# Kernel optimization log

Measured on AMD Instinct MI355X. Metric: run time of the kernel, lower is better.

## Reference

```python
import jax, jax.numpy as jnp
import numpy as np

B, T, J, D = 32, 1024, 128, 256

def setup_inputs() -> dict:
    key = jax.random.key(0)
    k1, k2, k3 = jax.random.split(key, 3)
    C = jax.random.normal(k1, (B, T, D), dtype=jnp.float32)
    Q = jax.random.normal(k2, (B, J, D), dtype=jnp.float32)
    w = jax.random.uniform(k3, (3 * D,), dtype=jnp.float32)  # torch.rand(d_model*3)
    return {"C": C, "Q": Q, "w": w}


def reference(C, Q, w):
    d = C.shape[-1]
    # AttentionFlowLayer: w^T [h; u; h*u] computed as streaming weighted sum
    # (avoids materializing the (b,t,j,3d) concat tensor; same math)
    w_h, w_u, w_hu = w[:d], w[d:2 * d], w[2 * d:]
    S = ((C @ w_h)[:, :, None]                         # (b,t,1)
         + (Q @ w_u)[:, None, :]                       # (b,1,j)
         + jnp.einsum('btd,bjd->btj', C * w_hu, Q))    # (b,t,j)

    S_j = jax.nn.softmax(S, axis=2)  # softmax over query dim j
    S_t = jax.nn.softmax(S, axis=1)  # softmax over context dim t

    # Context2Query
    A = jnp.einsum('btj,bjd->btd', S_j, Q)
    # DCNAttention: S_j @ S_t^T @ C, associated as S_j @ (S_t^T @ C) for efficiency
    tmp = jnp.einsum('bsj,bsd->bjd', S_t, C)           # (b,j,d)
    Bm = jnp.einsum('btj,bjd->btd', S_j, tmp)          # (b,t,d)

    # droprate = 0.0 -> dropout is identity
    return jnp.concatenate((C, A, C * A, C * Bm), axis=2)  # (b,t,4d)
```

## Files before the change

kernel.cpp:

```cpp
#include <hip/hip_runtime.h>
#include <math.h>

#define BB 32
#define TT 1024
#define JJ 128
#define DD 256

typedef unsigned short u16;
typedef short s16x8 __attribute__((ext_vector_type(8)));
typedef float f32x4 __attribute__((ext_vector_type(4)));

#define MFMA_BF16(a, b, c) __builtin_amdgcn_mfma_f32_16x16x32_bf16((a), (b), (c), 0, 0, 0)

__device__ inline u16 f2bf(float f) {
    unsigned int u = __float_as_uint(f);
    u += 0x7FFFu + ((u >> 16) & 1u);
    return (u16)(u >> 16);
}
__device__ inline float bf2f(u16 h) {
    return __uint_as_float(((unsigned int)h) << 16);
}

__global__ __launch_bounds__(256) void k_qprep(const float* __restrict__ Q,
                                               const float* __restrict__ w,
                                               float* __restrict__ qu,
                                               u16* __restrict__ Qhi,
                                               u16* __restrict__ Qlo,
                                               u16* __restrict__ Qt) {
    const int b = blockIdx.x >> 1, jh = blockIdx.x & 1;
    const int tid = threadIdx.x;
    __shared__ float sW[256];
    __shared__ __align__(16) u16 sTr[256 * 72];
    sW[tid] = w[DD + tid];
    __syncthreads();
    const int jj = tid >> 2, s = tid & 3;
    const int j = jh * 64 + jj;
    const float* qp = Q + ((size_t)b * JJ + j) * DD + s * 64;
    u16* hp = Qhi + ((size_t)b * JJ + j) * DD + s * 64;
    u16* lp = Qlo + ((size_t)b * JJ + j) * DD + s * 64;
    float dot = 0.f;
    #pragma unroll
    for (int q = 0; q < 16; q++) {
        float4 v = *(const float4*)(qp + q * 4);
        const float* wq = &sW[s * 64 + q * 4];
        dot += v.x * wq[0] + v.y * wq[1] + v.z * wq[2] + v.w * wq[3];
        ushort4 h, l;
        h.x = f2bf(v.x); l.x = f2bf(v.x - bf2f(h.x));
        h.y = f2bf(v.y); l.y = f2bf(v.y - bf2f(h.y));
        h.z = f2bf(v.z); l.z = f2bf(v.z - bf2f(h.z));
        h.w = f2bf(v.w); l.w = f2bf(v.w - bf2f(h.w));
        *(ushort4*)(hp + q * 4) = h;
        *(ushort4*)(lp + q * 4) = l;
        int d = s * 64 + q * 4;
        sTr[(d + 0) * 72 + jj] = h.x;
        sTr[(d + 1) * 72 + jj] = h.y;
        sTr[(d + 2) * 72 + jj] = h.z;
        sTr[(d + 3) * 72 + jj] = h.w;
    }
    dot += __shfl_xor(dot, 1, 64);
    dot += __shfl_xor(dot, 2, 64);
    if (s == 0) qu[b * JJ + j] = dot;
    __syncthreads();
    const u16* srow = &sTr[tid * 72];
    u16* drow = &Qt[((size_t)b * DD + tid) * JJ + jh * 64];
    #pragma unroll
    for (int q = 0; q < 8; q++) *(uint4*)&drow[q * 8] = *(const uint4*)&srow[q * 8];
}

__global__ __launch_bounds__(256) void k_S(const float* __restrict__ C,
                                           const u16* __restrict__ Qhi,
                                           const u16* __restrict__ Qlo,
                                           const float* __restrict__ w,
                                           const float* __restrict__ qu,
                                           u16* __restrict__ Xg,
                                           u16* __restrict__ Xt,
                                           u16* __restrict__ Cbf,
                                           float* __restrict__ rowmax,
                                           float* __restrict__ rowrcp,
                                           float* __restrict__ pm,
                                           float* __restrict__ ps) {
    const int id = blockIdx.x;
    const int b  = id & 31;
    const int bx = id >> 5;
    const int t0 = bx * 64;
    const int tid = threadIdx.x;

    union SMem {
        struct { u16 Ah[64 * 72]; u16 Al[64 * 72]; u16 Bh[128 * 72]; u16 Bl[128 * 72]; } g;
        struct { float S[64 * 132]; float RM[64]; float W[4]; float ER[64]; float PS2[256]; } e;
    };
    __shared__ __align__(16) SMem sm;
    __shared__ float sCH[64];
    __shared__ float sQU[128];

    if (tid < 128) sQU[tid] = qu[b * JJ + tid];

    const float* whu = w + 2 * DD;
    const float* Cb  = C + ((size_t)b * TT + t0) * DD;

    const int lane = tid & 63, wv = tid >> 6;
    const int wm = wv >> 1, wn = wv & 1;
    const int lr = lane & 15, lg = lane >> 4;

    f32x4 zero4 = {0.f, 0.f, 0.f, 0.f};
    f32x4 acc[2][4];
    #pragma unroll
    for (int m = 0; m < 2; m++)
        #pragma unroll
        for (int n = 0; n < 4; n++) acc[m][n] = zero4;

    const int tA = tid >> 2, sA = (tid & 3) * 16;
    const int jB = tid >> 1, sB = (tid & 1) * 32;
    float chdot = 0.f;

    for (int kc = 0; kc < DD; kc += 64) {
        __syncthreads();
        {
            const float* cp  = Cb + (size_t)tA * DD + kc + sA;
            const float* wp  = whu + kc + sA;
            const float* whp = w + kc + sA;
            float cc[16], ww[16], wh[16];
            #pragma unroll
            for (int q = 0; q < 4; q++) {
                *(float4*)&cc[q * 4] = *(const float4*)(cp + q * 4);
                *(float4*)&ww[q * 4] = *(const float4*)(wp + q * 4);
                *(float4*)&wh[q * 4] = *(const float4*)(whp + q * 4);
            }
            u16 hi16[16], lo16[16], cb16[16];
            #pragma unroll
            for (int u = 0; u < 16; u++) {
                chdot += cc[u] * wh[u];
                cb16[u] = f2bf(cc[u]);
                float v = cc[u] * ww[u];
                u16 h = f2bf(v);
                hi16[u] = h;
                lo16[u] = f2bf(v - bf2f(h));
            }
            u16* cbp = &Cbf[((size_t)b * TT + t0 + tA) * DD + kc + sA];
            *(uint4*)&cbp[0] = *(uint4*)&cb16[0];
            *(uint4*)&cbp[8] = *(uint4*)&cb16[8];
            int o = tA * 72 + sA;
            *(uint4*)&sm.g.Ah[o]     = *(uint4*)&hi16[0];
            *(uint4*)&sm.g.Ah[o + 8] = *(uint4*)&hi16[8];
            *(uint4*)&sm.g.Al[o]     = *(uint4*)&lo16[0];
            *(uint4*)&sm.g.Al[o + 8] = *(uint4*)&lo16[8];
        }
        {
            const uint4* qh = (const uint4*)&Qhi[((size_t)b * JJ + jB) * DD + kc + sB];
            const uint4* ql = (const uint4*)&Qlo[((size_t)b * JJ + jB) * DD + kc + sB];
            uint4* dh = (uint4*)&sm.g.Bh[jB * 72 + sB];
            uint4* dl = (uint4*)&sm.g.Bl[jB * 72 + sB];
            #pragma unroll
            for (int q = 0; q < 4; q++) { dh[q] = qh[q]; dl[q] = ql[q]; }
        }
        __syncthreads();
        #pragma unroll
        for (int ks = 0; ks < 2; ks++) {
            const int ko = ks * 32 + lg * 8;
            s16x8 ah[2], al[2], bh[4], bl[4];
            #pragma unroll
            for (int m = 0; m < 2; m++) {
                ah[m] = *(const s16x8*)&sm.g.Ah[(wm * 32 + m * 16 + lr) * 72 + ko];
                al[m] = *(const s16x8*)&sm.g.Al[(wm * 32 + m * 16 + lr) * 72 + ko];
            }
            #pragma unroll
            for (int n = 0; n < 4; n++) {
                bh[n] = *(const s16x8*)&sm.g.Bh[(wn * 64 + n * 16 + lr) * 72 + ko];
                bl[n] = *(const s16x8*)&sm.g.Bl[(wn * 64 + n * 16 + lr) * 72 + ko];
            }
            #pragma unroll
            for (int m = 0; m < 2; m++)
                #pragma unroll
                for (int n = 0; n < 4; n++) {
                    f32x4 t = acc[m][n];
                    t = MFMA_BF16(ah[m], bh[n], t);
                    t = MFMA_BF16(ah[m], bl[n], t);
                    t = MFMA_BF16(al[m], bh[n], t);
                    acc[m][n] = t;
                }
        }
    }

    chdot += __shfl_xor(chdot, 1, 64);
    chdot += __shfl_xor(chdot, 2, 64);
    if ((tid & 3) == 0) sCH[tid >> 2] = chdot;

    __syncthreads();
    #pragma unroll
    for (int m = 0; m < 2; m++) {
        int row0 = wm * 32 + m * 16 + lg * 4;
        #pragma unroll
        for (int n = 0; n < 4; n++) {
            int col = wn * 64 + n * 16 + lr;
            float qv = sQU[col];
            #pragma unroll
            for (int reg = 0; reg < 4; reg++)
                sm.e.S[(row0 + reg) * 132 + col] = acc[m][n][reg] + sCH[row0 + reg] + qv;
        }
    }
    __syncthreads();
    {
        int r = tid >> 2, s = tid & 3;
        float v[32];
        float* Sr = &sm.e.S[r * 132 + s * 32];
        #pragma unroll
        for (int q = 0; q < 8; q++) *(float4*)&v[q * 4] = *(const float4*)&Sr[q * 4];
        float mx = v[0];
        #pragma unroll
        for (int u = 1; u < 32; u++) mx = fmaxf(mx, v[u]);
        mx = fmaxf(mx, __shfl_xor(mx, 1, 64));
        mx = fmaxf(mx, __shfl_xor(mx, 2, 64));
        float sum = 0.f;
        #pragma unroll
        for (int u = 0; u < 32; u++) { v[u] = __expf(v[u] - mx); sum += v[u]; }
        sum += __shfl_xor(sum, 1, 64);
        sum += __shfl_xor(sum, 2, 64);
        #pragma unroll
        for (int q = 0; q < 8; q++) *(float4*)&Sr[q * 4] = *(const float4*)&v[q * 4];
        u16 xp[32];
        #pragma unroll
        for (int u = 0; u < 32; u++) xp[u] = f2bf(v[u]);
        u16* xgp = &Xg[((size_t)b * TT + t0 + r) * JJ + s * 32];
        #pragma unroll
        for (int q = 0; q < 4; q++) *(uint4*)&xgp[q * 8] = *(uint4*)&xp[q * 8];
        if (s == 0) {
            sm.e.RM[r] = mx;
            rowmax[(size_t)b * TT + t0 + r] = mx;
            rowrcp[(size_t)b * TT + t0 + r] = 1.0f / sum;
        }
        float wmx = mx;
        wmx = fmaxf(wmx, __shfl_xor(wmx, 4, 64));
        wmx = fmaxf(wmx, __shfl_xor(wmx, 8, 64));
        wmx = fmaxf(wmx, __shfl_xor(wmx, 16, 64));
        wmx = fmaxf(wmx, __shfl_xor(wmx, 32, 64));
        if (lane == 0) sm.e.W[wv] = wmx;
    }
    __syncthreads();
    const float Mb = fmaxf(fmaxf(sm.e.W[0], sm.e.W[1]), fmaxf(sm.e.W[2], sm.e.W[3]));
    if (tid < 64) sm.e.ER[tid] = __expf(sm.e.RM[tid] - Mb);
    {
        int j = tid & 127, seg = tid >> 7;
        u16 xb[32];
        #pragma unroll
        for (int k = 0; k < 32; k++)
            xb[k] = f2bf(sm.e.S[(seg * 32 + k) * 132 + j]);
        u16* xtp = &Xt[((size_t)b * JJ + j) * TT + t0 + seg * 32];
        #pragma unroll
        for (int q = 0; q < 4; q++) *(uint4*)&xtp[q * 8] = *(uint4*)&xb[q * 8];
    }
    __syncthreads();
    {
        int j = tid & 127, h = tid >> 7;
        float cs = 0.f;
        #pragma unroll
        for (int k = 0; k < 32; k++)
            cs = fmaf(sm.e.S[(h * 32 + k) * 132 + j], sm.e.ER[h * 32 + k], cs);
        sm.e.PS2[h * 128 + j] = cs;
    }
    __syncthreads();
    if (tid < 128) ps[((size_t)b * 16 + bx) * JJ + tid] = sm.e.PS2[tid] + sm.e.PS2[128 + tid];
    if (tid == 0)  pm[b * 16 + bx] = Mb;
}

__global__ __launch_bounds__(256) void k_tmp(const u16* __restrict__ Xt,
                                             const u16* __restrict__ Cbf,
                                             const float* __restrict__ rowmax,
                                             const float* __restrict__ pm,
                                             const float* __restrict__ ps,
                                             u16* __restrict__ Tt) {
    const int id = blockIdx.x;
    const int b = id & 31, dh = id >> 5;
    const int d0 = dh * 32;
    const int tid = threadIdx.x;
    __shared__ __align__(16) u16 sG[128 * 72];
    __shared__ __align__(16) u16 sCt[32 * 72];
    __shared__ float sER[1024];
    __shared__ float sEC[128];
    __shared__ float sPE[16];
    __shared__ float sW2[4];
    const int lane = tid & 63, wv = tid >> 6;

    {
        float4 rm4 = *(const float4*)&rowmax[(size_t)b * TT + tid * 4];
        float km = fmaxf(fmaxf(rm4.x, rm4.y), fmaxf(rm4.z, rm4.w));
        #pragma unroll
        for (int off = 1; off < 64; off <<= 1) km = fmaxf(km, __shfl_xor(km, off, 64));
        if (lane == 0) sW2[wv] = km;
        __syncthreads();
        const float K = fmaxf(fmaxf(sW2[0], sW2[1]), fmaxf(sW2[2], sW2[3]));
        float4 e4;
        e4.x = __expf(rm4.x - K);
        e4.y = __expf(rm4.y - K);
        e4.z = __expf(rm4.z - K);
        e4.w = __expf(rm4.w - K);
        *(float4*)&sER[tid * 4] = e4;
        if (tid < 16) sPE[tid] = __expf(pm[b * 16 + tid] - K);
        __syncthreads();
        if (tid < 128) {
            float cy = 0.f;
            #pragma unroll
            for (int blk = 0; blk < 16; blk++)
                cy = fmaf(ps[((size_t)b * 16 + blk) * JJ + tid], sPE[blk], cy);
            sEC[tid] = 1.0f / cy;
        }
    }

    const int lr = lane & 15, lg = lane >> 4;
    f32x4 zero4 = {0.f, 0.f, 0.f, 0.f};
    f32x4 acc[2][2];
    acc[0][0] = zero4; acc[0][1] = zero4; acc[1][0] = zero4; acc[1][1] = zero4;

    const int gj = tid >> 1, gs = (tid & 1) * 32;
    const int ct = tid & 63, cg = (tid >> 6) * 8;

    for (int tt = 0; tt < TT; tt += 64) {
        __syncthreads();
        {
            const u16* xtp = &Xt[((size_t)b * JJ + gj) * TT + tt + gs];
            u16* gp = &sG[gj * 72 + gs];
            #pragma unroll
            for (int q = 0; q < 4; q++) *(uint4*)&gp[q * 8] = *(const uint4*)&xtp[q * 8];
        }
        {
            float e = sER[tt + ct];
            uint4 cv = *(const uint4*)&Cbf[((size_t)b * TT + tt + ct) * DD + d0 + cg];
            const u16* cp = (const u16*)&cv;
            #pragma unroll
            for (int u = 0; u < 8; u++) sCt[(cg + u) * 72 + ct] = f2bf(bf2f(cp[u]) * e);
        }
        __syncthreads();
        #pragma unroll
        for (int ks = 0; ks < 2; ks++) {
            int ko = ks * 32 + lg * 8;
            s16x8 a0 = *(const s16x8*)&sG[(wv * 32 + lr) * 72 + ko];
            s16x8 a1 = *(const s16x8*)&sG[(wv * 32 + 16 + lr) * 72 + ko];
            s16x8 b0 = *(const s16x8*)&sCt[(lr) * 72 + ko];
            s16x8 b1 = *(const s16x8*)&sCt[(16 + lr) * 72 + ko];
            acc[0][0] = MFMA_BF16(a0, b0, acc[0][0]);
            acc[0][1] = MFMA_BF16(a0, b1, acc[0][1]);
            acc[1][0] = MFMA_BF16(a1, b0, acc[1][0]);
            acc[1][1] = MFMA_BF16(a1, b1, acc[1][1]);
        }
    }
    #pragma unroll
    for (int mr = 0; mr < 2; mr++)
        #pragma unroll
        for (int nr = 0; nr < 2; nr++)
            #pragma unroll
            for (int reg = 0; reg < 4; reg++) {
                int j = wv * 32 + mr * 16 + lg * 4 + reg;
                int d = d0 + nr * 16 + lr;
                Tt[((size_t)b * DD + d) * JJ + j] = f2bf(acc[mr][nr][reg] * sEC[j]);
            }
}

__global__ __launch_bounds__(256) void k_out(const u16* __restrict__ Xg,
                                             const u16* __restrict__ Qt,
                                             const u16* __restrict__ Tt,
                                             const u16* __restrict__ Cbf,
                                             const float* __restrict__ rowrcp,
                                             float* __restrict__ out) {
    const int id = blockIdx.x;
    const int b = id & 31, k = id >> 5;
    const int dc = k & 3, tc = k >> 2;
    const int t0 = tc * 64, d0 = dc * 64;
    const int tid = threadIdx.x;
    __shared__ __align__(16) u16 sX[64 * 136];
    __shared__ __align__(16) u16 sQ[64 * 136];
    __shared__ __align__(16) u16 sT[64 * 136];
    const size_t xbase = ((size_t)b * TT + t0) * JJ;
    const size_t qbase = ((size_t)b * DD + d0) * JJ;
    #pragma unroll
    for (int i = 0; i < 4; i++) {
        int c = tid + 256 * i;
        int row = c >> 4, col = (c & 15) * 8;
        int lo = row * 136 + col;
        *(uint4*)&sX[lo] = *(const uint4*)&Xg[xbase + (size_t)row * JJ + col];
        *(uint4*)&sQ[lo] = *(const uint4*)&Qt[qbase + (size_t)row * JJ + col];
        *(uint4*)&sT[lo] = *(const uint4*)&Tt[qbase + (size_t)row * JJ + col];
    }
    __syncthreads();
    const int lane = tid & 63, wv = tid >> 6;
    const int wm = wv >> 1, wn = wv & 1;
    const int lr = lane & 15, lg = lane >> 4;
    f32x4 zero4 = {0.f, 0.f, 0.f, 0.f};
    f32x4 accA[2][2], accB[2][2];
    #pragma unroll
    for (int mr = 0; mr < 2; mr++)
        #pragma unroll
        for (int nr = 0; nr < 2; nr++) { accA[mr][nr] = zero4; accB[mr][nr] = zero4; }

    #pragma unroll
    for (int ks = 0; ks < 4; ks++) {
        int kc = ks * 32 + lg * 8;
        s16x8 a0 = *(const s16x8*)&sX[(wm * 32 + lr) * 136 + kc];
        s16x8 a1 = *(const s16x8*)&sX[(wm * 32 + 16 + lr) * 136 + kc];
        s16x8 q0 = *(const s16x8*)&sQ[(wn * 32 + lr) * 136 + kc];
        s16x8 q1 = *(const s16x8*)&sQ[(wn * 32 + 16 + lr) * 136 + kc];
        s16x8 u0 = *(const s16x8*)&sT[(wn * 32 + lr) * 136 + kc];
        s16x8 u1 = *(const s16x8*)&sT[(wn * 32 + 16 + lr) * 136 + kc];
        accA[0][0] = MFMA_BF16(a0, q0, accA[0][0]);
        accA[0][1] = MFMA_BF16(a0, q1, accA[0][1]);
        accA[1][0] = MFMA_BF16(a1, q0, accA[1][0]);
        accA[1][1] = MFMA_BF16(a1, q1, accA[1][1]);
        accB[0][0] = MFMA_BF16(a0, u0, accB[0][0]);
        accB[0][1] = MFMA_BF16(a0, u1, accB[0][1]);
        accB[1][0] = MFMA_BF16(a1, u0, accB[1][0]);
        accB[1][1] = MFMA_BF16(a1, u1, accB[1][1]);
    }

    #pragma unroll
    for (int mr = 0; mr < 2; mr++) {
        #pragma unroll
        for (int reg = 0; reg < 4; reg++) {
            int t = t0 + wm * 32 + mr * 16 + lg * 4 + reg;
            float r = rowrcp[(size_t)b * TT + t];
            const u16* Cp = Cbf + ((size_t)b * TT + t) * DD;
            float* op = out + ((size_t)b * TT + t) * (4 * DD);
            #pragma unroll
            for (int nr = 0; nr < 2; nr++) {
                int d = d0 + wn * 32 + nr * 16 + lr;
                float cv = bf2f(Cp[d]);
                float av = accA[mr][nr][reg] * r;
                float bv = accB[mr][nr][reg] * r;
                op[d]          = cv;
                op[DD + d]     = av;
                op[2 * DD + d] = cv * av;
                op[3 * DD + d] = cv * bv;
            }
        }
    }
}

extern "C" void kernel_launch(void* const* d_in, const int* in_sizes, int n_in,
                              void* d_out, int out_size, void* d_ws, size_t ws_size,
                              hipStream_t stream) {
    const float* C = (const float*)d_in[0];
    const float* Q = (const float*)d_in[1];
    const float* w = (const float*)d_in[2];
    float* out = (float*)d_out;
    float* p = (float*)d_ws;

    u16* Xg  = (u16*)p;     p += (size_t)BB * TT * JJ / 2;
    u16* Xt  = (u16*)p;     p += (size_t)BB * JJ * TT / 2;
    u16* Cbf = (u16*)p;     p += (size_t)BB * TT * DD / 2;
    u16* Qt  = (u16*)p;     p += (size_t)BB * DD * JJ / 2;
    u16* Qhi = (u16*)p;     p += (size_t)BB * JJ * DD / 2;
    u16* Qlo = (u16*)p;     p += (size_t)BB * JJ * DD / 2;
    u16* Tt  = (u16*)p;     p += (size_t)BB * DD * JJ / 2;
    float* qu     = p;      p += BB * JJ;
    float* rowmax = p;      p += BB * TT;
    float* rowrcp = p;      p += BB * TT;
    float* pm     = p;      p += BB * 16;
    float* ps     = p;      p += (size_t)BB * 16 * JJ;

    k_qprep <<<dim3(BB * 2), dim3(256), 0, stream>>>(Q, w, qu, Qhi, Qlo, Qt);
    k_S     <<<dim3(16 * BB), dim3(256), 0, stream>>>(C, Qhi, Qlo, w, qu, Xg, Xt, Cbf, rowmax, rowrcp, pm, ps);
    k_tmp   <<<dim3(8 * BB), dim3(256), 0, stream>>>(Xt, Cbf, rowmax, pm, ps, Tt);
    k_out   <<<dim3(64 * BB), dim3(256), 0, stream>>>(Xg, Qt, Tt, Cbf, rowrcp, out);
}
```

Measured before the change: 84.53 us.

## Fuse Q preprocessing kernel into S kernel, recomputing splits per block

Removes the separate k_qprep launch. Each k_S block now loads fp32 Q directly, computes the bf16 hi/lo split and the Q·w_u dot product itself, and blocks with bx==kc/64 write their slice of the transposed bf16 Qt. This saves one kernel launch and the global round-trip of Qhi/Qlo/qu. In exchange every one of the 16 t-blocks per batch redundantly converts the full Q tile and reads fp32 instead of bf16 pairs. The Qt transpose read from LDS is strided and may hit bank conflicts.

```diff
diff --git a/kernel.cpp b/kernel.cpp
--- a/kernel.cpp
+++ b/kernel.cpp
@@ -21,60 +21,13 @@
     return __uint_as_float(((unsigned int)h) << 16);
 }
 
-__global__ __launch_bounds__(256) void k_qprep(const float* __restrict__ Q,
-                                               const float* __restrict__ w,
-                                               float* __restrict__ qu,
-                                               u16* __restrict__ Qhi,
-                                               u16* __restrict__ Qlo,
-                                               u16* __restrict__ Qt) {
-    const int b = blockIdx.x >> 1, jh = blockIdx.x & 1;
-    const int tid = threadIdx.x;
-    __shared__ float sW[256];
-    __shared__ __align__(16) u16 sTr[256 * 72];
-    sW[tid] = w[DD + tid];
-    __syncthreads();
-    const int jj = tid >> 2, s = tid & 3;
-    const int j = jh * 64 + jj;
-    const float* qp = Q + ((size_t)b * JJ + j) * DD + s * 64;
-    u16* hp = Qhi + ((size_t)b * JJ + j) * DD + s * 64;
-    u16* lp = Qlo + ((size_t)b * JJ + j) * DD + s * 64;
-    float dot = 0.f;
-    #pragma unroll
-    for (int q = 0; q < 16; q++) {
-        float4 v = *(const float4*)(qp + q * 4);
-        const float* wq = &sW[s * 64 + q * 4];
-        dot += v.x * wq[0] + v.y * wq[1] + v.z * wq[2] + v.w * wq[3];
-        ushort4 h, l;
-        h.x = f2bf(v.x); l.x = f2bf(v.x - bf2f(h.x));
-        h.y = f2bf(v.y); l.y = f2bf(v.y - bf2f(h.y));
-        h.z = f2bf(v.z); l.z = f2bf(v.z - bf2f(h.z));
-        h.w = f2bf(v.w); l.w = f2bf(v.w - bf2f(h.w));
-        *(ushort4*)(hp + q * 4) = h;
-        *(ushort4*)(lp + q * 4) = l;
-        int d = s * 64 + q * 4;
-        sTr[(d + 0) * 72 + jj] = h.x;
-        sTr[(d + 1) * 72 + jj] = h.y;
-        sTr[(d + 2) * 72 + jj] = h.z;
-        sTr[(d + 3) * 72 + jj] = h.w;
-    }
-    dot += __shfl_xor(dot, 1, 64);
-    dot += __shfl_xor(dot, 2, 64);
-    if (s == 0) qu[b * JJ + j] = dot;
-    __syncthreads();
-    const u16* srow = &sTr[tid * 72];
-    u16* drow = &Qt[((size_t)b * DD + tid) * JJ + jh * 64];
-    #pragma unroll
-    for (int q = 0; q < 8; q++) *(uint4*)&drow[q * 8] = *(const uint4*)&srow[q * 8];
-}
-
 __global__ __launch_bounds__(256) void k_S(const float* __restrict__ C,
-                                           const u16* __restrict__ Qhi,
-                                           const u16* __restrict__ Qlo,
+                                           const float* __restrict__ Q,
                                            const float* __restrict__ w,
-                                           const float* __restrict__ qu,
                                            u16* __restrict__ Xg,
                                            u16* __restrict__ Xt,
                                            u16* __restrict__ Cbf,
+                                           u16* __restrict__ Qt,
                                            float* __restrict__ rowmax,
                                            float* __restrict__ rowrcp,
                                            float* __restrict__ pm,
@@ -93,10 +46,9 @@
     __shared__ float sCH[64];
     __shared__ float sQU[128];
 
-    if (tid < 128) sQU[tid] = qu[b * JJ + tid];
-
     const float* whu = w + 2 * DD;
     const float* Cb  = C + ((size_t)b * TT + t0) * DD;
+    const float* Qb  = Q + (size_t)b * JJ * DD;
 
     const int lane = tid & 63, wv = tid >> 6;
     const int wm = wv >> 1, wn = wv & 1;
@@ -112,6 +64,7 @@
     const int tA = tid >> 2, sA = (tid & 3) * 16;
     const int jB = tid >> 1, sB = (tid & 1) * 32;
     float chdot = 0.f;
+    float qdot  = 0.f;
 
     for (int kc = 0; kc < DD; kc += 64) {
         __syncthreads();
@@ -146,12 +99,26 @@
             *(uint4*)&sm.g.Al[o + 8] = *(uint4*)&lo16[8];
         }
         {
-            const uint4* qh = (const uint4*)&Qhi[((size_t)b * JJ + jB) * DD + kc + sB];
-            const uint4* ql = (const uint4*)&Qlo[((size_t)b * JJ + jB) * DD + kc + sB];
+            const float* qp  = Qb + (size_t)jB * DD + kc + sB;
+            const float* wup = w + DD + kc + sB;
+            float qq[32], wu[32];
+            #pragma unroll
+            for (int q = 0; q < 8; q++) {
+                *(float4*)&qq[q * 4] = *(const float4*)(qp + q * 4);
+                *(float4*)&wu[q * 4] = *(const float4*)(wup + q * 4);
+            }
+            u16 h16[32], l16[32];
+            #pragma unroll
+            for (int u = 0; u < 32; u++) {
+                qdot += qq[u] * wu[u];
+                u16 h = f2bf(qq[u]);
+                h16[u] = h;
+                l16[u] = f2bf(qq[u] - bf2f(h));
+            }
             uint4* dh = (uint4*)&sm.g.Bh[jB * 72 + sB];
             uint4* dl = (uint4*)&sm.g.Bl[jB * 72 + sB];
             #pragma unroll
-            for (int q = 0; q < 4; q++) { dh[q] = qh[q]; dl[q] = ql[q]; }
+            for (int q = 0; q < 4; q++) { dh[q] = *(uint4*)&h16[q * 8]; dl[q] = *(uint4*)&l16[q * 8]; }
         }
         __syncthreads();
         #pragma unroll
@@ -179,11 +146,23 @@
                     acc[m][n] = t;
                 }
         }
+        if (bx == (kc >> 6)) {
+            int dloc = tid >> 2;
+            int j0 = (tid & 3) * 32;
+            u16 qb[32];
+            #pragma unroll
+            for (int u = 0; u < 32; u++) qb[u] = sm.g.Bh[(j0 + u) * 72 + dloc];
+            u16* qtp = &Qt[((size_t)b * DD + kc + dloc) * JJ + j0];
+            #pragma unroll
+            for (int q = 0; q < 4; q++) *(uint4*)&qtp[q * 8] = *(uint4*)&qb[q * 8];
+        }
     }
 
     chdot += __shfl_xor(chdot, 1, 64);
     chdot += __shfl_xor(chdot, 2, 64);
     if ((tid & 3) == 0) sCH[tid >> 2] = chdot;
+    float qd = qdot + __shfl_xor(qdot, 1, 64);
+    if ((tid & 1) == 0) sQU[tid >> 1] = qd;
 
     __syncthreads();
     #pragma unroll
@@ -445,17 +424,13 @@
     u16* Xt  = (u16*)p;     p += (size_t)BB * JJ * TT / 2;
     u16* Cbf = (u16*)p;     p += (size_t)BB * TT * DD / 2;
     u16* Qt  = (u16*)p;     p += (size_t)BB * DD * JJ / 2;
-    u16* Qhi = (u16*)p;     p += (size_t)BB * JJ * DD / 2;
-    u16* Qlo = (u16*)p;     p += (size_t)BB * JJ * DD / 2;
     u16* Tt  = (u16*)p;     p += (size_t)BB * DD * JJ / 2;
-    float* qu     = p;      p += BB * JJ;
     float* rowmax = p;      p += BB * TT;
     float* rowrcp = p;      p += BB * TT;
     float* pm     = p;      p += BB * 16;
     float* ps     = p;      p += (size_t)BB * 16 * JJ;
 
-    k_qprep <<<dim3(BB * 2), dim3(256), 0, stream>>>(Q, w, qu, Qhi, Qlo, Qt);
-    k_S     <<<dim3(16 * BB), dim3(256), 0, stream>>>(C, Qhi, Qlo, w, qu, Xg, Xt, Cbf, rowmax, rowrcp, pm, ps);
+    k_S     <<<dim3(16 * BB), dim3(256), 0, stream>>>(C, Q, w, Xg, Xt, Cbf, Qt, rowmax, rowrcp, pm, ps);
     k_tmp   <<<dim3(8 * BB), dim3(256), 0, stream>>>(Xt, Cbf, rowmax, pm, ps, Tt);
     k_out   <<<dim3(64 * BB), dim3(256), 0, stream>>>(Xg, Qt, Tt, Cbf, rowrcp, out);
 }
```

Measured after the change: 82.02 us. 1.03x faster.
